# Performance work log

Hardware: AMD Instinct MI355X
Metric: run time of the kernel (lower is better)

## Reference

```python
import jax, jax.numpy as jnp
import numpy as np
from jax.scipy.special import gammaln

N, F, P = 65536, 256, 4194304
PARAM_RES = 1e-12          # param_resolution_scale
W_MODEL = 1.0              # weight_model_bits
EPS = float(np.finfo(np.float32).eps * 5)
HALF_LOG2_2PIE = 0.5 * float(np.log2(2.0 * np.pi * np.e))
LAMBDA_BITS = 2.0 * float(np.log2(100.0))
LN2 = float(np.log(2.0))


def nanmedian(x):
    """torch.nanmedian semantics for 1-D x: lower median of finite values; nan if none."""
    finite = jnp.isfinite(x)
    m = finite.sum()
    xs = jnp.sort(jnp.where(finite, x, jnp.inf))
    idx = jnp.maximum((m - 1) // 2, 0)
    med = xs[idx]
    return jnp.where(m == 0, jnp.nan, med)


def feature_resolution(x):
    """Median positive gap between sorted finite values, clamped to [1e-12, 0.1]."""
    finite = jnp.isfinite(x)
    xs = jnp.sort(jnp.where(finite, x, jnp.inf))
    diffs = xs[1:] - xs[:-1]
    pos = jnp.where(diffs > 1e-12, diffs, jnp.nan)
    res = nanmedian(pos)
    valid = jnp.where(jnp.isfinite(res), res, 1e-6)
    final = jnp.clip(valid, 1e-12, 0.1)
    return jnp.where(finite.sum() < 2, jnp.asarray(1e-6, x.dtype), final)


def feature_bits(y, log_jac, resolution):
    finite = jnp.isfinite(y)
    n_f = finite.sum().astype(y.dtype)
    n = jnp.asarray(y.size, y.dtype)
    n_ex = n - n_f
    yc = jnp.where(finite, y, 0.0)
    mean = yc.sum() / jnp.maximum(n_f, 1.0)
    sq = jnp.where(finite, (y - mean) ** 2, 0.0)
    var = jnp.maximum(sq.sum() / jnp.maximum(n_f, 1.0), 1e-12)
    diff_bits = jnp.where(n_f > 1, n_f * (HALF_LOG2_2PIE + 0.5 * jnp.log2(var)), 0.0)
    lj_sum = jnp.where(finite, log_jac, 0.0).sum() / LN2
    lj_bits = jnp.where(n_f > 0, lj_sum, 0.0)
    ex_bits = jnp.where(n_ex > 0, n_ex * jnp.log2(1.0 / resolution), 0.0)
    has_partial = (n_ex > 0) & (n_ex < n)
    log_binom = jnp.where(
        has_partial,
        gammaln(n + 1.0) - gammaln(n_ex + 1.0) - gammaln(n - n_ex + 1.0),
        0.0,
    )
    part_bits = jnp.where(has_partial, log_binom / LN2, 0.0)
    return diff_bits + lj_bits + ex_bits + part_bits + LAMBDA_BITS


def two_param_yeo_johnson(x, lam1, lam2):
    """x:[N], lam1/lam2 scalars -> (y:[N], log_jac:[N])."""
    pos = x >= 0
    xp = jnp.where(pos, x, 0.0)           # safe input for positive branch
    xn = jnp.where(pos, 0.0, x)           # safe input for negative branch
    l1z = jnp.abs(lam1) < EPS
    l1s = jnp.where(l1z, 1.0, lam1)       # avoid div-by-zero in unselected branch
    lp = jnp.log1p(xp)
    y_pos = jnp.where(l1z, lp, ((1.0 + xp) ** l1s - 1.0) / l1s)
    lj_pos = jnp.where(l1z, -lp, (lam1 - 1.0) * lp)
    l2t = jnp.abs(lam2 - 2.0) < EPS
    two_m = jnp.where(l2t, 1.0, 2.0 - lam2)
    base = jnp.maximum(1.0 - xn, 1e-18)
    ln = jnp.log1p(-xn)
    y_neg = jnp.where(l2t, -ln, -((base ** two_m - 1.0) / two_m))
    lj_neg = jnp.where(l2t, -ln, (1.0 - lam2) * jnp.log(base))
    y = jnp.where(pos, y_pos, y_neg)
    lj = jnp.where(pos, lj_pos, lj_neg)
    return y, lj


def _feature_total_bits(x_col, lam1, lam2, rp):
    """One SA step for one feature: evaluate current + 5 proposals, pick best, emit bits.
    (feature_complexity in the original is computed but unused -> omitted.)"""
    res = feature_resolution(x_col)  # depends only on x_col; shared by all proposals
    std_dev = 0.1  # 0.1 * temperature(=1.0)
    all_l1 = jnp.concatenate([lam1[None], lam1 + std_dev * rp[0::2]])  # [6]
    all_l2 = jnp.concatenate([lam2[None], lam2 + std_dev * rp[1::2]])  # [6]

    def score(l1, l2):
        y, lj = two_param_yeo_johnson(x_col, l1, l2)
        return feature_bits(y, lj, res)

    scores = jax.vmap(score)(all_l1, all_l2)  # [6]
    mn = scores.min()
    w = (scores == mn).astype(x_col.dtype)
    tw = jnp.maximum(w.sum(), 1e-8)
    best_l1 = (all_l1 * w).sum() / tw
    best_l2 = (all_l2 * w).sum() / tw
    y, lj = two_param_yeo_johnson(x_col, best_l1, best_l2)
    return feature_bits(y, lj, res)


def setup_inputs() -> dict:
    key = jax.random.key(0)
    k1, k2, k3 = jax.random.split(key, 3)
    return {
        "x": jax.random.normal(k1, (N, F), dtype=jnp.float32),
        "lam1": jnp.ones((F,), dtype=jnp.float32),
        "lam2": jnp.ones((F,), dtype=jnp.float32),
        "random_proposals": jax.random.normal(k2, (F, 10), dtype=jnp.float32),
        "params": jax.random.normal(k3, (P,), dtype=jnp.float32),
    }


def reference(x, lam1, lam2, random_proposals, params):
    # data bits: per-feature SA pipeline, vmapped over features
    per_feat = jax.vmap(_feature_total_bits)(x.T, lam1, lam2, random_proposals)  # [F]
    data_bits = per_feat.sum()
    # model bits: parameter tensor as a feature with fixed resolution, zero log-Jacobian
    model_bits = feature_bits(params, jnp.zeros_like(params), jnp.asarray(PARAM_RES, params.dtype))
    return data_bits + W_MODEL * model_bits
```

## Files before the change

kernel.cpp:

```cpp
#include <hip/hip_runtime.h>
#include <math.h>

#define NFEAT 256
#define NROWS 65536
#define PCOUNT 4194304
#define PBLK 64
#define CH2 512
#define RGRP 4
#define NSLOT 28
#define F_EPS 5.9604645e-07f
#define F_LN2 0.69314718056f
#define DELTA_MAX 0.45f

#define FAST_LOG2(v) __builtin_log2f(v)
#define FAST_EXP2(v) __builtin_exp2f(v)

constexpr double D_HALF_LOG2_2PIE = 0.5 * 2.8378770664093453 / 0.6931471805599453;
constexpr double D_LAMBDA_BITS = 13.287712379549449;

__device__ inline double wave_reduce_add(double v) {
  for (int o = 32; o > 0; o >>= 1) v += __shfl_down(v, o, 64);
  return v;
}

__device__ inline double horner_exp(const double* m, double d) {
  double p = m[5] * (1.0 / 120.0);
  p = p * d + m[4] * (1.0 / 24.0);
  p = p * d + m[3] * (1.0 / 6.0);
  p = p * d + m[2] * 0.5;
  p = p * d + m[1];
  p = p * d + m[0];
  return p;
}

__global__ __launch_bounds__(512, 8) void k_pass1(
    const float* __restrict__ x, const float* __restrict__ lam1,
    const float* __restrict__ lam2, const float* __restrict__ rp,
    const float* __restrict__ params, float* __restrict__ P1,
    double* __restrict__ pPart, int nyj, int rpt)
{
  const int tid = threadIdx.x;

  if ((int)blockIdx.x >= nyj) {
    __shared__ double lred[2][8];
    const int b = blockIdx.x - nyj;
    const float4* p4 = (const float4*)params;
    double s = 0.0, q = 0.0;
    for (int i = b * 512 + tid; i < PCOUNT / 4; i += PBLK * 512) {
      float4 v = p4[i];
      s += (double)v.x + (double)v.y + (double)v.z + (double)v.w;
      q += (double)v.x * v.x + (double)v.y * v.y
         + (double)v.z * v.z + (double)v.w * v.w;
    }
    s = wave_reduce_add(s); q = wave_reduce_add(q);
    const int w = tid >> 6;
    if ((tid & 63) == 0) { lred[0][w] = s; lred[1][w] = q; }
    __syncthreads();
    if (tid == 0) {
      double S = 0.0, Q = 0.0;
#pragma unroll
      for (int i = 0; i < 8; ++i) { S += lred[0][i]; Q += lred[1][i]; }
      pPart[2 * b]     = S;
      pPart[2 * b + 1] = Q;
    }
    return;
  }

  const int f = tid & 255;
  const int sub = tid >> 8;
  const int c = blockIdx.x * 2 + sub;
  __shared__ float red[NSLOT][NFEAT];
  __shared__ int bad;
  if (tid == 0) bad = 0;
  __syncthreads();

  const float L1 = lam1[f], L2 = lam2[f];
  const float An = 2.0f - L2;
  {
    bool b = (fabsf(L1) < F_EPS) || (fabsf(An) < F_EPS);
#pragma unroll
    for (int j = 1; j < 6; ++j) {
      float dp = 0.1f * rp[f * 10 + 2 * (j - 1)];
      float dn = -0.1f * rp[f * 10 + 2 * (j - 1) + 1];
      b = b || (fabsf(L1 + dp) < F_EPS) || (fabsf(An + dn) < F_EPS)
            || (fabsf(dp) > DELTA_MAX) || (fabsf(dn) > DELTA_MAX);
    }
    if (b) bad = 1;
  }
  __syncthreads();

  const float* xp = x + (size_t)c * rpt * NFEAT + f;
  float out[NSLOT];

  if (bad == 0) {
    float Mp[6], Mp2[6], Mn[6], Mn2[6];
#pragma unroll
    for (int k = 0; k < 6; ++k) { Mp[k] = 0.f; Mp2[k] = 0.f; Mn[k] = 0.f; Mn2[k] = 0.f; }
    float u2p = 0.f, u2a = 0.f, npos = 0.f;

#pragma unroll 4
    for (int i = 0; i < rpt; ++i) {
      const float v = xp[(size_t)i * NFEAT];
      const bool pos = v >= 0.0f;
      const float u = FAST_LOG2(1.0f + fabsf(v));
      u2a += u;
      u2p += pos ? u : 0.0f;
      npos += pos ? 1.0f : 0.0f;
      const float q = u * F_LN2;
      const float B = FAST_EXP2((pos ? L1 : An) * u);
      const float B2 = B * B;
      const float Bp = pos ? B : 0.0f;
      const float Bn = B - Bp;
      const float Cp = pos ? B2 : 0.0f;
      const float Cn = B2 - Cp;
      Mp[0] += Bp; Mp2[0] += Cp; Mn[0] += Bn; Mn2[0] += Cn;
      float qk = q;
      Mp[1] = fmaf(Bp, qk, Mp[1]); Mp2[1] = fmaf(Cp, qk, Mp2[1]);
      Mn[1] = fmaf(Bn, qk, Mn[1]); Mn2[1] = fmaf(Cn, qk, Mn2[1]);
#pragma unroll
      for (int k = 2; k < 6; ++k) {
        qk *= q;
        Mp[k] = fmaf(Bp, qk, Mp[k]); Mp2[k] = fmaf(Cp, qk, Mp2[k]);
        Mn[k] = fmaf(Bn, qk, Mn[k]); Mn2[k] = fmaf(Cn, qk, Mn2[k]);
      }
    }
#pragma unroll
    for (int k = 0; k < 6; ++k) {
      out[k]      = Mp[k];
      out[6 + k]  = Mp2[k];
      out[12 + k] = Mn[k];
      out[18 + k] = Mn2[k];
    }
    out[24] = u2p; out[25] = u2a; out[26] = npos; out[27] = 0.0f;
  } else {
    float ga_p[6], ga_n[6], gs_p[6], gs_n[6], gt_p[6], gt_n[6];
#pragma unroll
    for (int j = 0; j < 6; ++j) {
      float dp = (j == 0) ? 0.0f : 0.1f * rp[f * 10 + 2 * (j - 1)];
      float dn = (j == 0) ? 0.0f : -0.1f * rp[f * 10 + 2 * (j - 1) + 1];
      float a1 = L1 + dp;
      float a2 = An + dn;
      bool z1 = fabsf(a1) < F_EPS;
      bool z2 = fabsf(a2) < F_EPS;
      ga_p[j] = z1 ? 0.0f : a1;
      gs_p[j] = z1 ? 0.0f : 1.0f / a1;
      gt_p[j] = z1 ? F_LN2 : 0.0f;
      ga_n[j] = z2 ? 0.0f : a2;
      gs_n[j] = z2 ? 0.0f : -1.0f / a2;
      gt_n[j] = z2 ? -F_LN2 : 0.0f;
    }
    float as[6], aq[6];
#pragma unroll
    for (int j = 0; j < 6; ++j) { as[j] = 0.f; aq[j] = 0.f; }
    float u2p = 0.f, u2a = 0.f;
    for (int i = 0; i < rpt; ++i) {
      float v = xp[(size_t)i * NFEAT];
      bool pos = v >= 0.0f;
      float u2 = FAST_LOG2(1.0f + fabsf(v));
      u2a += u2;
      u2p += pos ? u2 : 0.0f;
#pragma unroll
      for (int j = 0; j < 6; ++j) {
        float a  = pos ? ga_p[j] : ga_n[j];
        float s  = pos ? gs_p[j] : gs_n[j];
        float tt = pos ? gt_p[j] : gt_n[j];
        float e = FAST_EXP2(a * u2);
        float y = fmaf(tt, u2, fmaf(s, e, -s));
        as[j] += y;
        aq[j] = fmaf(y, y, aq[j]);
      }
    }
#pragma unroll
    for (int k = 0; k < NSLOT; ++k) out[k] = 0.0f;
#pragma unroll
    for (int j = 0; j < 6; ++j) { out[j] = as[j]; out[6 + j] = aq[j]; }
    out[24] = u2p; out[25] = u2a; out[26] = 0.0f; out[27] = 1.0f;
  }

  if (sub == 1) {
#pragma unroll
    for (int k = 0; k < NSLOT; ++k) red[k][f] = out[k];
  }
  __syncthreads();
  if (sub == 0) {
#pragma unroll
    for (int k = 0; k < NSLOT; ++k)
      P1[((size_t)blockIdx.x * NSLOT + k) * NFEAT + f] = out[k] + red[k][f];
  }
}

__global__ __launch_bounds__(256) void k_reduce_S(
    const float* __restrict__ P1, double* __restrict__ S2, int nsets)
{
  const int k = blockIdx.x / RGRP;
  const int cg = blockIdx.x % RGRP;
  const int f = threadIdx.x;
  const int per = nsets / RGRP;
  const int c0 = cg * per;
  double a0 = 0.0, a1 = 0.0, a2 = 0.0, a3 = 0.0;
  for (int c = c0; c < c0 + per; c += 4) {
    a0 += (double)P1[((size_t)(c + 0) * NSLOT + k) * NFEAT + f];
    a1 += (double)P1[((size_t)(c + 1) * NSLOT + k) * NFEAT + f];
    a2 += (double)P1[((size_t)(c + 2) * NSLOT + k) * NFEAT + f];
    a3 += (double)P1[((size_t)(c + 3) * NSLOT + k) * NFEAT + f];
  }
  S2[((size_t)k * RGRP + cg) * NFEAT + f] = (a0 + a1) + (a2 + a3);
}

__global__ __launch_bounds__(256) void k_pick(
    const double* __restrict__ S2, const float* __restrict__ lam1,
    const float* __restrict__ lam2, const float* __restrict__ rp,
    float* __restrict__ bestL, int* __restrict__ tied,
    double* __restrict__ bitsF, int* __restrict__ anyTied)
{
  const int f = threadIdx.x;
  if (f == 0) *anyTied = 0;
  double s[NSLOT];
#pragma unroll
  for (int k = 0; k < NSLOT; ++k) {
    double a = 0.0;
#pragma unroll
    for (int cg = 0; cg < RGRP; ++cg)
      a += S2[((size_t)k * RGRP + cg) * NFEAT + f];
    s[k] = a;
  }
  const double n = (double)NROWS;
  const bool direct = s[27] > 0.5;
  const double npos = s[26];
  const double nneg = n - npos;
  const double sup = s[24];
  const double sun = s[25] - s[24];
  const float L1 = lam1[f], L2 = lam2[f];
  const double dAn = 2.0 - (double)L2;
  double scores[6], al1[6], al2[6];
#pragma unroll
  for (int j = 0; j < 6; ++j) {
    float l1 = (j == 0) ? L1 : L1 + 0.1f * rp[f * 10 + 2 * (j - 1)];
    float l2 = (j == 0) ? L2 : L2 + 0.1f * rp[f * 10 + 2 * (j - 1) + 1];
    al1[j] = (double)l1; al2[j] = (double)l2;
    bool z1 = fabsf(l1) < F_EPS;
    bool z2 = fabsf(l2 - 2.0f) < F_EPS;
    double ccp = z1 ? -1.0 : (double)l1 - 1.0;
    double ccn = z2 ? -1.0 : 1.0 - (double)l2;
    double ljb = ccp * sup + ccn * sun;

    double sum_y, sum_y2;
    if (direct) {
      sum_y  = s[j];
      sum_y2 = s[6 + j];
    } else {
      const double dp  = (double)l1 - (double)L1;
      const double dnn = (2.0 - (double)l2) - dAn;
      const double sp = 1.0 / ((double)L1 + dp);
      const double sn = -1.0 / (dAn + dnn);
      const double Ep  = horner_exp(&s[0],  dp);
      const double Ep2 = horner_exp(&s[6],  2.0 * dp);
      const double En  = horner_exp(&s[12], dnn);
      const double En2 = horner_exp(&s[18], 2.0 * dnn);
      sum_y  = sp * (Ep - npos) + sn * (En - nneg);
      sum_y2 = sp * sp * (Ep2 - 2.0 * Ep + npos)
             + sn * sn * (En2 - 2.0 * En + nneg);
    }
    double mean = sum_y / n;
    double var = sum_y2 / n - mean * mean;
    var = var > 1e-12 ? var : 1e-12;
    scores[j] = n * (D_HALF_LOG2_2PIE + 0.5 * log2(var)) + ljb + D_LAMBDA_BITS;
  }
  double mn = scores[0];
#pragma unroll
  for (int j = 1; j < 6; ++j) mn = scores[j] < mn ? scores[j] : mn;
  double wsum = 0.0, b1 = 0.0, b2 = 0.0;
#pragma unroll
  for (int j = 0; j < 6; ++j) {
    double w = (scores[j] == mn) ? 1.0 : 0.0;
    wsum += w; b1 += w * al1[j]; b2 += w * al2[j];
  }
  bestL[2 * f]     = (float)(b1 / wsum);
  bestL[2 * f + 1] = (float)(b2 / wsum);
  const int isTied = (wsum > 1.5) ? 1 : 0;
  tied[f] = isTied;
  if (isTied) atomicOr(anyTied, 1);
  bitsF[f] = mn;
}

__global__ __launch_bounds__(256) void k_pass2(
    const float* __restrict__ x, const float* __restrict__ bestL,
    const int* __restrict__ anyTied, float* __restrict__ P2)
{
  if (*anyTied == 0) return;
  const int t = threadIdx.x;
  const int c = blockIdx.x;
  const int rpt = NROWS / CH2;
  const float l1 = bestL[2 * t], l2 = bestL[2 * t + 1];
  const bool z1 = fabsf(l1) < F_EPS;
  const bool z2 = fabsf(l2 - 2.0f) < F_EPS;
  const float tm = 2.0f - l2;
  const float a_p = z1 ? 0.f : l1,  s_pv = z1 ? 0.f : 1.f / l1,  t_pv = z1 ? F_LN2 : 0.f;
  const float a_n = z2 ? 0.f : tm,  s_nv = z2 ? 0.f : -1.f / tm, t_nv = z2 ? -F_LN2 : 0.f;

  float sy = 0.f, sq = 0.f;
  const float* xp = x + (size_t)c * rpt * NFEAT + t;
  for (int i = 0; i < rpt; ++i) {
    float v = xp[(size_t)i * NFEAT];
    bool pos = v >= 0.0f;
    float u2 = FAST_LOG2(1.0f + fabsf(v));
    float a  = pos ? a_p : a_n;
    float s  = pos ? s_pv : s_nv;
    float tt = pos ? t_pv : t_nv;
    float e = FAST_EXP2(a * u2);
    float y = fmaf(tt, u2, fmaf(s, e, -s));
    sy += y;
    sq = fmaf(y, y, sq);
  }
  P2[((size_t)c * 2 + 0) * NFEAT + t] = sy;
  P2[((size_t)c * 2 + 1) * NFEAT + t] = sq;
}

__global__ __launch_bounds__(64) void k_featbits(
    const float* __restrict__ P1, const float* __restrict__ P2,
    const float* __restrict__ bestL, const int* __restrict__ tied,
    double* __restrict__ bitsF, int nsets)
{
  const int f = blockIdx.x;
  if (!tied[f]) return;
  const int lane = threadIdx.x;
  double s0 = 0.0, s1 = 0.0, sup = 0.0, sua = 0.0;
  for (int c = lane; c < CH2; c += 64) {
    s0 += (double)P2[((size_t)c * 2 + 0) * NFEAT + f];
    s1 += (double)P2[((size_t)c * 2 + 1) * NFEAT + f];
  }
  for (int c = lane; c < nsets; c += 64) {
    sup += (double)P1[((size_t)c * NSLOT + 24) * NFEAT + f];
    sua += (double)P1[((size_t)c * NSLOT + 25) * NFEAT + f];
  }
  s0 = wave_reduce_add(s0); s1 = wave_reduce_add(s1);
  sup = wave_reduce_add(sup); sua = wave_reduce_add(sua);
  if (lane == 0) {
    const float l1 = bestL[2 * f], l2 = bestL[2 * f + 1];
    bool z1 = fabsf(l1) < F_EPS;
    bool z2 = fabsf(l2 - 2.0f) < F_EPS;
    double ccp = z1 ? -1.0 : (double)l1 - 1.0;
    double ccn = z2 ? -1.0 : 1.0 - (double)l2;
    double ljb = ccp * sup + ccn * (sua - sup);
    const double n = (double)NROWS;
    double mean = s0 / n;
    double var = s1 / n - mean * mean;
    var = var > 1e-12 ? var : 1e-12;
    bitsF[f] = n * (D_HALF_LOG2_2PIE + 0.5 * log2(var)) + ljb + D_LAMBDA_BITS;
  }
}

__global__ __launch_bounds__(256) void k_final(
    const double* __restrict__ bitsF, const double* __restrict__ pPart,
    float* __restrict__ out)
{
  __shared__ double l[4], lp[4], lq[4];
  const int t = threadIdx.x;
  double s  = bitsF[t];
  double sp = (t < PBLK) ? pPart[2 * t]     : 0.0;
  double sq = (t < PBLK) ? pPart[2 * t + 1] : 0.0;
  s = wave_reduce_add(s); sp = wave_reduce_add(sp); sq = wave_reduce_add(sq);
  const int w = t >> 6;
  if ((t & 63) == 0) { l[w] = s; lp[w] = sp; lq[w] = sq; }
  __syncthreads();
  if (t == 0) {
    double data = l[0] + l[1] + l[2] + l[3];
    double S = lp[0] + lp[1] + lp[2] + lp[3];
    double Q = lq[0] + lq[1] + lq[2] + lq[3];
    const double n = (double)PCOUNT;
    double mean = S / n;
    double var = Q / n - mean * mean;
    var = var > 1e-12 ? var : 1e-12;
    double model = n * (D_HALF_LOG2_2PIE + 0.5 * log2(var)) + D_LAMBDA_BITS;
    out[0] = (float)(data + model);
  }
}

extern "C" void kernel_launch(void* const* d_in, const int* in_sizes, int n_in,
                              void* d_out, int out_size, void* d_ws, size_t ws_size,
                              hipStream_t stream)
{
  const float* x      = (const float*)d_in[0];
  const float* lam1   = (const float*)d_in[1];
  const float* lam2   = (const float*)d_in[2];
  const float* rp     = (const float*)d_in[3];
  const float* params = (const float*)d_in[4];

  char* ws = (char*)d_ws;
  double* pPart = (double*)ws;
  float*  bestL = (float*)(ws + 1024);
  double* bitsF = (double*)(ws + 3072);
  int*    tied  = (int*)(ws + 5120);
  int*    anyT  = (int*)(ws + 6144);
  double* S2    = (double*)(ws + 6176);
  float*  P1    = (float*)(ws + 235552);

  int nsets = 512;
  while (nsets > 64) {
    size_t need = 235552 + (size_t)nsets * NSLOT * NFEAT * 4
                         + (size_t)CH2 * 2 * NFEAT * 4;
    if (need <= ws_size) break;
    nsets >>= 1;
  }
  float* P2 = (float*)(ws + 235552 + (size_t)nsets * NSLOT * NFEAT * 4);
  int rpt = NROWS / (2 * nsets);

  k_pass1<<<nsets + PBLK, 512, 0, stream>>>(x, lam1, lam2, rp, params, P1,
                                            pPart, nsets, rpt);
  k_reduce_S<<<NSLOT * RGRP, 256, 0, stream>>>(P1, S2, nsets);
  k_pick<<<1, 256, 0, stream>>>(S2, lam1, lam2, rp, bestL, tied, bitsF, anyT);
  k_pass2<<<CH2, 256, 0, stream>>>(x, bestL, anyT, P2);
  k_featbits<<<NFEAT, 64, 0, stream>>>(P1, P2, bestL, tied, bitsF, nsets);
  k_final<<<1, 256, 0, stream>>>(bitsF, pPart, (float*)d_out);
}
```

Baseline: 59.30 us.

## Fuse per-block partial reduction into pass1 via double atomics, drop reduce kernel

Each pass1 block now folds its two half-block partials in shared memory and atomically adds its 28x256 slot sums into a global double buffer. This removes the P1 partial array write/readback and the separate k_reduce_S launch, and lets k_pick and k_featbits read totals directly. In exchange it adds a memset launch and 512 blocks each issuing 7168 double atomicAdds onto the same addresses, which may contend. Summation order also becomes nondeterministic.

```diff
diff --git a/kernel.cpp b/kernel.cpp
--- a/kernel.cpp
+++ b/kernel.cpp
@@ -6,7 +6,6 @@
 #define PCOUNT 4194304
 #define PBLK 64
 #define CH2 512
-#define RGRP 4
 #define NSLOT 28
 #define F_EPS 5.9604645e-07f
 #define F_LN2 0.69314718056f
@@ -36,7 +35,7 @@
 __global__ __launch_bounds__(512, 8) void k_pass1(
     const float* __restrict__ x, const float* __restrict__ lam1,
     const float* __restrict__ lam2, const float* __restrict__ rp,
-    const float* __restrict__ params, float* __restrict__ P1,
+    const float* __restrict__ params, double* __restrict__ S2f,
     double* __restrict__ pPart, int nyj, int rpt)
 {
   const int tid = threadIdx.x;
@@ -184,31 +183,15 @@
   __syncthreads();
   if (sub == 0) {
 #pragma unroll
-    for (int k = 0; k < NSLOT; ++k)
-      P1[((size_t)blockIdx.x * NSLOT + k) * NFEAT + f] = out[k] + red[k][f];
-  }
-}
-
-__global__ __launch_bounds__(256) void k_reduce_S(
-    const float* __restrict__ P1, double* __restrict__ S2, int nsets)
-{
-  const int k = blockIdx.x / RGRP;
-  const int cg = blockIdx.x % RGRP;
-  const int f = threadIdx.x;
-  const int per = nsets / RGRP;
-  const int c0 = cg * per;
-  double a0 = 0.0, a1 = 0.0, a2 = 0.0, a3 = 0.0;
-  for (int c = c0; c < c0 + per; c += 4) {
-    a0 += (double)P1[((size_t)(c + 0) * NSLOT + k) * NFEAT + f];
-    a1 += (double)P1[((size_t)(c + 1) * NSLOT + k) * NFEAT + f];
-    a2 += (double)P1[((size_t)(c + 2) * NSLOT + k) * NFEAT + f];
-    a3 += (double)P1[((size_t)(c + 3) * NSLOT + k) * NFEAT + f];
-  }
-  S2[((size_t)k * RGRP + cg) * NFEAT + f] = (a0 + a1) + (a2 + a3);
+    for (int k = 0; k < NSLOT; ++k) red[k][f] += out[k];
+  }
+  __syncthreads();
+  for (int idx = tid; idx < NSLOT * NFEAT; idx += 512)
+    atomicAdd(&S2f[idx], (double)red[idx >> 8][idx & 255]);
 }
 
 __global__ __launch_bounds__(256) void k_pick(
-    const double* __restrict__ S2, const float* __restrict__ lam1,
+    const double* __restrict__ S2f, const float* __restrict__ lam1,
     const float* __restrict__ lam2, const float* __restrict__ rp,
     float* __restrict__ bestL, int* __restrict__ tied,
     double* __restrict__ bitsF, int* __restrict__ anyTied)
@@ -217,13 +200,7 @@
   if (f == 0) *anyTied = 0;
   double s[NSLOT];
 #pragma unroll
-  for (int k = 0; k < NSLOT; ++k) {
-    double a = 0.0;
-#pragma unroll
-    for (int cg = 0; cg < RGRP; ++cg)
-      a += S2[((size_t)k * RGRP + cg) * NFEAT + f];
-    s[k] = a;
-  }
+  for (int k = 0; k < NSLOT; ++k) s[k] = S2f[k * NFEAT + f];
   const double n = (double)NROWS;
   const bool direct = s[27] > 0.5;
   const double npos = s[26];
@@ -317,25 +294,22 @@
 }
 
 __global__ __launch_bounds__(64) void k_featbits(
-    const float* __restrict__ P1, const float* __restrict__ P2,
+    const double* __restrict__ S2f, const float* __restrict__ P2,
     const float* __restrict__ bestL, const int* __restrict__ tied,
-    double* __restrict__ bitsF, int nsets)
+    double* __restrict__ bitsF)
 {
   const int f = blockIdx.x;
   if (!tied[f]) return;
   const int lane = threadIdx.x;
-  double s0 = 0.0, s1 = 0.0, sup = 0.0, sua = 0.0;
+  double s0 = 0.0, s1 = 0.0;
   for (int c = lane; c < CH2; c += 64) {
     s0 += (double)P2[((size_t)c * 2 + 0) * NFEAT + f];
     s1 += (double)P2[((size_t)c * 2 + 1) * NFEAT + f];
   }
-  for (int c = lane; c < nsets; c += 64) {
-    sup += (double)P1[((size_t)c * NSLOT + 24) * NFEAT + f];
-    sua += (double)P1[((size_t)c * NSLOT + 25) * NFEAT + f];
-  }
   s0 = wave_reduce_add(s0); s1 = wave_reduce_add(s1);
-  sup = wave_reduce_add(sup); sua = wave_reduce_add(sua);
   if (lane == 0) {
+    const double sup = S2f[24 * NFEAT + f];
+    const double sua = S2f[25 * NFEAT + f];
     const float l1 = bestL[2 * f], l2 = bestL[2 * f + 1];
     bool z1 = fabsf(l1) < F_EPS;
     bool z2 = fabsf(l2 - 2.0f) < F_EPS;
@@ -387,29 +361,22 @@
   const float* params = (const float*)d_in[4];
 
   char* ws = (char*)d_ws;
-  double* pPart = (double*)ws;
-  float*  bestL = (float*)(ws + 1024);
-  double* bitsF = (double*)(ws + 3072);
-  int*    tied  = (int*)(ws + 5120);
-  int*    anyT  = (int*)(ws + 6144);
-  double* S2    = (double*)(ws + 6176);
-  float*  P1    = (float*)(ws + 235552);
-
-  int nsets = 512;
-  while (nsets > 64) {
-    size_t need = 235552 + (size_t)nsets * NSLOT * NFEAT * 4
-                         + (size_t)CH2 * 2 * NFEAT * 4;
-    if (need <= ws_size) break;
-    nsets >>= 1;
-  }
-  float* P2 = (float*)(ws + 235552 + (size_t)nsets * NSLOT * NFEAT * 4);
-  int rpt = NROWS / (2 * nsets);
-
-  k_pass1<<<nsets + PBLK, 512, 0, stream>>>(x, lam1, lam2, rp, params, P1,
-                                            pPart, nsets, rpt);
-  k_reduce_S<<<NSLOT * RGRP, 256, 0, stream>>>(P1, S2, nsets);
-  k_pick<<<1, 256, 0, stream>>>(S2, lam1, lam2, rp, bestL, tied, bitsF, anyT);
+  double* S2f   = (double*)ws;
+  double* pPart = (double*)(ws + 57344);
+  float*  bestL = (float*)(ws + 58368);
+  double* bitsF = (double*)(ws + 60416);
+  int*    tied  = (int*)(ws + 62464);
+  int*    anyT  = (int*)(ws + 63488);
+  float*  P2    = (float*)(ws + 63520);
+
+  const int nyj = 512;
+  const int rpt = NROWS / (2 * nyj);
+
+  (void)hipMemsetAsync(S2f, 0, NSLOT * NFEAT * sizeof(double), stream);
+  k_pass1<<<nyj + PBLK, 512, 0, stream>>>(x, lam1, lam2, rp, params, S2f,
+                                          pPart, nyj, rpt);
+  k_pick<<<1, 256, 0, stream>>>(S2f, lam1, lam2, rp, bestL, tied, bitsF, anyT);
   k_pass2<<<CH2, 256, 0, stream>>>(x, bestL, anyT, P2);
-  k_featbits<<<NFEAT, 64, 0, stream>>>(P1, P2, bestL, tied, bitsF, nsets);
+  k_featbits<<<NFEAT, 64, 0, stream>>>(S2f, P2, bestL, tied, bitsF);
   k_final<<<1, 256, 0, stream>>>(bitsF, pPart, (float*)d_out);
 }
```

New measurement: 64.76 us. 1.09x slower.
